# Kernel tuning notes

Hardware: AMD Instinct MI355X
Metric: run time of the kernel (lower is better)

## Reference

```python
import jax, jax.numpy as jnp
import numpy as np

TAU = 2.0      # LIF membrane time constant
V_TH = 1.0     # firing threshold (spikingjelly default)
NUM_HEADS = 8

@jax.custom_vjp
def heaviside(x, alpha):
    return (x >= 0.0).astype(x.dtype)

def _hv_fwd(x, alpha):
    return heaviside(x, alpha), (x, alpha)

def _hv_bwd(res, g):
    x, alpha = res
    s = jax.nn.sigmoid(alpha * x)  # sigmoid surrogate gradient
    return (g * alpha * s * (1.0 - s), jnp.zeros_like(alpha))

heaviside.defvjp(_hv_fwd, _hv_bwd)

def lif(x_seq, alpha):
    """Multi-step LIF over leading time dim. Hard reset to 0, detach_reset."""
    def step(v, x):
        h = v + (x - v) / TAU
        s = heaviside(h - V_TH, alpha)
        v_new = h * (1.0 - jax.lax.stop_gradient(s))
        return v_new, s
    _, spikes = jax.lax.scan(step, jnp.zeros_like(x_seq[0]), x_seq)
    return spikes

def bn1d(x, gamma, beta, mean, var, eps=1e-5):
    # x: [TB, C, N]; inference-mode BatchNorm1d over channel dim
    inv = gamma / jnp.sqrt(var + eps)
    return x * inv[None, :, None] + (beta - mean * inv)[None, :, None]

def setup_inputs():
    T, B, C, H, W = 4, 32, 384, 16, 16
    key = jax.random.key(0)
    ks = jax.random.split(key, 6)
    w = lambda k: jax.random.normal(k, (C, C), jnp.float32) * (1.0 / np.sqrt(C))
    ones = jnp.ones((C,), jnp.float32)
    zeros = jnp.zeros((C,), jnp.float32)
    return dict(
        x=jax.random.normal(ks[0], (T, B, C, H, W), jnp.float32),
        alpha=jnp.float32(2.0),
        q_w=w(ks[1]), q_gamma=ones, q_beta=zeros, q_mean=zeros, q_var=ones,
        k_w=w(ks[2]), k_gamma=ones, k_beta=zeros, k_mean=zeros, k_var=ones,
        v_w=w(ks[3]), v_gamma=ones, v_beta=zeros, v_mean=zeros, v_var=ones,
        proj_w=w(ks[4]), proj_b=jax.random.normal(ks[5], (C,), jnp.float32) * 0.01,
        p_gamma=ones, p_beta=zeros, p_mean=zeros, p_var=ones,
    )

def reference(x, alpha, q_w, q_gamma, q_beta, q_mean, q_var,
              k_w, k_gamma, k_beta, k_mean, k_var,
              v_w, v_gamma, v_beta, v_mean, v_var,
              proj_w, proj_b, p_gamma, p_beta, p_mean, p_var):
    T, B, C, H, W = x.shape
    N = H * W
    d = C // NUM_HEADS

    s = lif(x, alpha).reshape(T, B, C, N)         # proj_lif + flatten(3)
    xf = s.reshape(T * B, C, N)                   # flatten(0,1)

    def branch(w_, g_, b_, m_, v_):
        y = jnp.einsum('oc,bcn->bon', w_, xf)     # conv1x1
        y = bn1d(y, g_, b_, m_, v_).reshape(T, B, C, N)
        y = lif(y, alpha)
        # [T,B,C,N] -> [T,B,N,C] -> [T,B,N,h,d] -> [T,B,h,N,d]
        return y.transpose(0, 1, 3, 2).reshape(T, B, N, NUM_HEADS, d).transpose(0, 1, 3, 2, 4)

    q = branch(q_w, q_gamma, q_beta, q_mean, q_var)
    k = branch(k_w, k_gamma, k_beta, k_mean, k_var)
    v = branch(v_w, v_gamma, v_beta, v_mean, v_var)

    attn = jnp.einsum('tbhnd,tbhmd->tbhnm', q, k)          # q @ k^T (no softmax)
    out = jnp.einsum('tbhnm,tbhmd->tbhnd', attn, v) * 0.125
    # transpose(3,4) then reshape -> [T,B,C,N] (head-major channel layout)
    out = out.transpose(0, 1, 2, 4, 3).reshape(T, B, C, N)
    out = lif(out, alpha)                                  # attn_lif

    of = out.reshape(T * B, C, N)
    y = jnp.einsum('oc,bcn->bon', proj_w, of) + proj_b[None, :, None]
    y = bn1d(y, p_gamma, p_beta, p_mean, p_var)
    return y.reshape(T, B, C, H, W)
```

## Files before the change

### kernel.cpp

```cpp
#include <hip/hip_runtime.h>
#include <hip/hip_bf16.h>

#define T_  4
#define B_  32
#define C_  384
#define N_  256
#define NH_ 8
#define D_  48

typedef __attribute__((ext_vector_type(8))) short bf16x8;
typedef __attribute__((ext_vector_type(4))) float f32x4;

__device__ __forceinline__ float bf2f(unsigned short s) {
    return __uint_as_float(((unsigned int)s) << 16);
}
__device__ __forceinline__ unsigned short f2bf(float f) {
    __hip_bfloat16 h = __float2bfloat16(f);
    return __builtin_bit_cast(unsigned short, h);
}

__global__ __launch_bounds__(256) void k_wsplit(const float* __restrict__ w0,
                                                const float* __restrict__ w1,
                                                const float* __restrict__ w2,
                                                const float* __restrict__ w3,
                                                unsigned short* __restrict__ hi,
                                                unsigned short* __restrict__ lo) {
    const float* w = (blockIdx.y==0) ? w0 : (blockIdx.y==1) ? w1 : (blockIdx.y==2) ? w2 : w3;
    int g = blockIdx.x*256 + threadIdx.x;
    int otile = g / 768;
    int rem = g - otile*768;
    int lane = rem & 63;
    int o  = otile*16 + (lane & 15);
    int k0 = (rem >> 6)*32 + (lane >> 4)*8;
    const float* src = w + (size_t)o*C_ + k0;
    unsigned short h8[8], l8[8];
    #pragma unroll
    for (int j=0;j<8;++j) {
        float f = src[j];
        h8[j] = f2bf(f);
        l8[j] = f2bf(f - bf2f(h8[j]));
    }
    size_t dst = (size_t)blockIdx.y*147456 + (size_t)g*8;
    *(uint4*)(hi + dst) = *(uint4*)h8;
    *(uint4*)(lo + dst) = *(uint4*)l8;
}

__global__ __launch_bounds__(256) void k_lif1(const float* __restrict__ x,
                                              unsigned char* __restrict__ s0b) {
    __shared__ unsigned short Tt[64*72];
    const int tid = threadIdx.x;
    const int b  = blockIdx.x;
    const int c0 = blockIdx.y * 64;
    const int n0 = blockIdx.z * 64;
    const int ci = tid >> 2;
    const int nj = (tid & 3) * 16;
    float v[16];
    #pragma unroll
    for (int i=0;i<16;++i) v[i]=0.f;
    for (int t = 0; t < T_; ++t) {
        const float* xp = x + (((size_t)t*B_ + b)*C_ + c0 + ci)*N_ + n0 + nj;
        #pragma unroll
        for (int q=0;q<4;++q) {
            float4 f = *(const float4*)(xp + q*4);
            float e[4] = {f.x,f.y,f.z,f.w};
            #pragma unroll
            for (int j=0;j<4;++j) {
                int ii = q*4+j;
                float h = v[ii] + (e[j] - v[ii])*0.5f;
                bool sp = (h - 1.0f) >= 0.f;
                v[ii] = sp ? 0.f : h;
                Tt[(nj + ii)*72 + ci] = sp ? 0x3F80u : 0u;
            }
        }
        __syncthreads();
        #pragma unroll
        for (int half=0; half<2; ++half) {
            int e = tid + half*256;
            int nl = e >> 3, cbyte = e & 7;
            unsigned short tmp[8];
            *(uint4*)tmp = *(const uint4*)&Tt[nl*72 + cbyte*8];
            unsigned byte = 0;
            #pragma unroll
            for (int j=0;j<8;++j) byte |= (tmp[j] ? 1u : 0u) << j;
            int n = n0 + nl, c = c0 + cbyte*8;
            int ks = c >> 5, kc = (c >> 3) & 3;
            size_t dst = ((((size_t)(t*B_ + b)*16 + (n>>4))*12 + ks)*64) + kc*16 + (n & 15);
            s0b[dst] = (unsigned char)byte;
        }
        __syncthreads();
    }
}

struct Br2 {
    const unsigned short* whi[3];
    const unsigned short* wlo[3];
    const float *g[3], *be[3], *me[3], *va[3];
    unsigned char* outb[3];
};

__global__ __launch_bounds__(256, 2) void k_branch(const unsigned char* __restrict__ s0b, Br2 a) {
    __shared__ float Ep[32*132];
    __shared__ float BNi[128], BNo[128];
    __shared__ unsigned short LUT[2048];
    const int tid = threadIdx.x;
    const int z  = blockIdx.z;
    const int o0 = blockIdx.y * 128;
    const int bx = blockIdx.x;
    const int b  = bx >> 3;
    const int n0 = (bx & 7) * 32;
    const int g32 = n0 >> 5;
    const int w    = tid >> 6;
    const int lane = tid & 63;
    const int quad = lane >> 4;
    const int lc   = lane & 15;
    const unsigned short* __restrict__ Wgh = a.whi[z];
    const unsigned short* __restrict__ Wgl = a.wlo[z];

    #pragma unroll
    for (int j=0;j<8;++j) LUT[tid*8 + j] = ((tid >> j) & 1) ? 0x3F80u : 0u;
    if (tid < 128) {
        int o = o0 + tid;
        float inv = a.g[z][o] / sqrtf(a.va[z][o] + 1e-5f);
        BNi[tid] = inv;
        BNo[tid] = a.be[z][o] - a.me[z][o]*inv;
    }
    __syncthreads();

    const int base_ot = (o0 >> 4) + (w >> 1)*4;
    const unsigned short* pAh[4];
    const unsigned short* pAl[4];
    const unsigned char* pBY[4];
    #pragma unroll
    for (int mt=0;mt<4;++mt) {
        size_t off = (size_t)(base_ot + mt)*6144 + lane*8;
        pAh[mt] = Wgh + off;
        pAl[mt] = Wgl + off;
    }
    #pragma unroll
    for (int nt=0;nt<4;++nt) {
        int cb = (w&1)*64 + nt*16;
        int t = cb >> 5;
        int ntile = (n0 >> 4) + ((cb >> 4) & 1);
        pBY[nt] = s0b + ((size_t)(t*B_ + b)*16 + ntile)*768 + lane;
    }

    f32x4 acc[4][4];
    #pragma unroll
    for (int mt=0;mt<4;++mt)
        #pragma unroll
        for (int nt=0;nt<4;++nt) { acc[mt][nt][0]=0.f; acc[mt][nt][1]=0.f; acc[mt][nt][2]=0.f; acc[mt][nt][3]=0.f; }

    #pragma unroll
    for (int ks = 0; ks < 12; ++ks) {
        bf16x8 ah[4], al[4], bb[4];
        unsigned char byt[4];
        #pragma unroll
        for (int nt=0;nt<4;++nt) { byt[nt] = *(pBY[nt]); pBY[nt] += 64; }
        #pragma unroll
        for (int mt=0;mt<4;++mt) {
            ah[mt] = *(const bf16x8*)(pAh[mt]); pAh[mt] += 512;
            al[mt] = *(const bf16x8*)(pAl[mt]); pAl[mt] += 512;
        }
        #pragma unroll
        for (int nt=0;nt<4;++nt) bb[nt] = *(const bf16x8*)&LUT[(int)byt[nt]*8];
        #pragma unroll
        for (int mt=0;mt<4;++mt)
            #pragma unroll
            for (int nt=0;nt<4;++nt) {
                acc[mt][nt] = __builtin_amdgcn_mfma_f32_16x16x32_bf16(ah[mt], bb[nt], acc[mt][nt], 0,0,0);
                acc[mt][nt] = __builtin_amdgcn_mfma_f32_16x16x32_bf16(al[mt], bb[nt], acc[mt][nt], 0,0,0);
            }
    }

    unsigned char* outb = a.outb[z];
    for (int r = 0; r < 4; ++r) {
        __syncthreads();
        int erow = (w>>1)*16 + quad*4;
        #pragma unroll
        for (int nt=0;nt<4;++nt) {
            int col = (w&1)*64 + nt*16 + lc;
            Ep[(erow+0)*132 + col] = acc[r][nt][0];
            Ep[(erow+1)*132 + col] = acc[r][nt][1];
            Ep[(erow+2)*132 + col] = acc[r][nt][2];
            Ep[(erow+3)*132 + col] = acc[r][nt][3];
        }
        __syncthreads();
        if (tid < 128) {
            int orow = tid >> 2;
            int bidx = tid & 3;
            int oloc = ((orow & 16) ? 64 : 0) + r*16 + (orow & 15);
            int o = o0 + oloc;
            float inv = BNi[oloc], off = BNo[oloc];
            float v[8];
            #pragma unroll
            for (int j=0;j<8;++j) v[j]=0.f;
            #pragma unroll
            for (int t=0;t<4;++t) {
                float4 f0 = *(const float4*)&Ep[orow*132 + t*32 + bidx*8];
                float4 f1 = *(const float4*)&Ep[orow*132 + t*32 + bidx*8 + 4];
                float e[8] = {f0.x,f0.y,f0.z,f0.w,f1.x,f1.y,f1.z,f1.w};
                unsigned byte = 0;
                #pragma unroll
                for (int j=0;j<8;++j) {
                    float y = e[j]*inv + off;
                    float h = v[j] + (y - v[j])*0.5f;
                    bool sp = (h - 1.0f) >= 0.f;
                    v[j] = sp ? 0.f : h;
                    byte |= (sp ? 1u : 0u) << j;
                }
                outb[(((size_t)(t*B_ + b)*8 + g32)*C_ + o)*4 + bidx] = (unsigned char)byte;
            }
        }
    }
}

__global__ __launch_bounds__(256) void k_attn(const unsigned char* __restrict__ qb,
                                              const unsigned char* __restrict__ kb,
                                              const unsigned char* __restrict__ vb,
                                              unsigned char* __restrict__ s2b) {
    __shared__ unsigned short Qt[256*72];
    __shared__ unsigned short KtVb[48*72];
    __shared__ unsigned long long KB[192], VB[192], QB[192];
    const int tid = threadIdx.x;
    const int w = tid >> 6, lane = tid & 63, quad = lane >> 4, lc = lane & 15;
    const int bh = blockIdx.x;
    const int b  = bh >> 3, hh = bh & 7;

    *(uint4*)&Qt[tid*72 + 48] = make_uint4(0,0,0,0);
    *(uint4*)&Qt[tid*72 + 56] = make_uint4(0,0,0,0);
    if (tid < 48) {
        *(uint4*)&KtVb[tid*72 + 48] = make_uint4(0,0,0,0);
        *(uint4*)&KtVb[tid*72 + 56] = make_uint4(0,0,0,0);
    }

    float vst[4][3][4];
    #pragma unroll
    for (int j=0;j<4;++j)
        #pragma unroll
        for (int nt=0;nt<3;++nt)
            #pragma unroll
            for (int r=0;r<4;++r) vst[j][nt][r]=0.f;

    for (int t = 0; t < T_; ++t) {
        __syncthreads();
        if (tid < 192) {
            int dd = tid >> 2, w64 = tid & 3;
            size_t s0 = (((size_t)(t*B_ + b)*8 + 2*w64)*C_ + hh*D_ + dd)*4;
            size_t s1 = s0 + (size_t)C_*4;
            KB[tid] = (unsigned long long)*(const unsigned int*)(kb + s0)
                    | ((unsigned long long)*(const unsigned int*)(kb + s1) << 32);
            VB[tid] = (unsigned long long)*(const unsigned int*)(vb + s0)
                    | ((unsigned long long)*(const unsigned int*)(vb + s1) << 32);
            QB[tid] = (unsigned long long)*(const unsigned int*)(qb + s0)
                    | ((unsigned long long)*(const unsigned int*)(qb + s1) << 32);
        }
        __syncthreads();
        {
            int q64 = tid >> 6, sh = tid & 63;
            #pragma unroll
            for (int dd=0; dd<48; ++dd)
                Qt[tid*72 + dd] = ((QB[dd*4 + q64] >> sh) & 1ULL) ? 0x3F80u : 0u;
        }
        #pragma unroll
        for (int i=0;i<9;++i) {
            int p = tid + i*256;
            if (p < 2304) {
                int dd1 = p / 48, dd2 = p - dd1*48;
                const unsigned long long* kr = &KB[dd1*4];
                const unsigned long long* vr = &VB[dd2*4];
                int c = __popcll(kr[0]&vr[0]) + __popcll(kr[1]&vr[1])
                      + __popcll(kr[2]&vr[2]) + __popcll(kr[3]&vr[3]);
                KtVb[dd2*72 + dd1] = f2bf((float)c);
            }
        }
        __syncthreads();
        f32x4 acc2[4][3];
        #pragma unroll
        for (int j=0;j<4;++j)
            #pragma unroll
            for (int nt=0;nt<3;++nt) { acc2[j][nt][0]=0.f; acc2[j][nt][1]=0.f; acc2[j][nt][2]=0.f; acc2[j][nt][3]=0.f; }
        #pragma unroll
        for (int k2=0; k2<2; ++k2) {
            bf16x8 bfr[3];
            #pragma unroll
            for (int nt=0;nt<3;++nt)
                bfr[nt] = *(const bf16x8*)&KtVb[(nt*16 + lc)*72 + k2*32 + quad*8];
            #pragma unroll
            for (int j=0;j<4;++j) {
                bf16x8 af = *(const bf16x8*)&Qt[((w*4 + j)*16 + lc)*72 + k2*32 + quad*8];
                #pragma unroll
                for (int nt=0;nt<3;++nt)
                    acc2[j][nt] = __builtin_amdgcn_mfma_f32_16x16x32_bf16(af, bfr[nt], acc2[j][nt], 0,0,0);
            }
        }
        #pragma unroll
        for (int j=0;j<4;++j) {
            int nr = (w*4 + j)*16 + quad*4;
            #pragma unroll
            for (int nt=0;nt<3;++nt)
                #pragma unroll
                for (int r=0;r<4;++r) {
                    float y = acc2[j][nt][r]*0.125f;
                    float vv = vst[j][nt][r];
                    float h = vv + (y - vv)*0.5f;
                    bool s = (h - 1.0f) >= 0.f;
                    vst[j][nt][r] = s ? 0.f : h;
                    Qt[(nr + r)*72 + nt*16 + lc] = s ? 0x3F80u : 0u;
                }
        }
        __syncthreads();
        {
            #pragma unroll
            for (int c8=0; c8<6; ++c8) {
                unsigned short tmp[8];
                *(uint4*)tmp = *(const uint4*)&Qt[tid*72 + c8*8];
                unsigned byte = 0;
                #pragma unroll
                for (int j=0;j<8;++j) byte |= (tmp[j] ? 1u : 0u) << j;
                int ci = hh*6 + c8;
                int ks = ci >> 2, kc = ci & 3;
                size_t dst = ((((size_t)(t*B_ + b)*16 + (tid>>4))*12 + ks)*64) + kc*16 + (tid & 15);
                s2b[dst] = (unsigned char)byte;
            }
        }
    }
}

__global__ __launch_bounds__(256, 2) void k_proj(const unsigned char* __restrict__ s2b,
        const unsigned short* __restrict__ Wgh, const unsigned short* __restrict__ Wgl,
        const float* __restrict__ pb,
        const float* __restrict__ g, const float* __restrict__ be,
        const float* __restrict__ me, const float* __restrict__ va,
        float* __restrict__ out) {
    __shared__ float Ep[32*132];
    __shared__ float BNi[128], BNo[128];
    __shared__ unsigned short LUT[2048];
    const int tid = threadIdx.x;
    const int o0 = blockIdx.y * 128;
    const int bx = blockIdx.x;
    const int t  = bx >> 6;
    const int b  = (bx >> 1) & 31;
    const int n0 = (bx & 1) * 128;
    const int w    = tid >> 6;
    const int lane = tid & 63;
    const int quad = lane >> 4;
    const int lc   = lane & 15;

    #pragma unroll
    for (int j=0;j<8;++j) LUT[tid*8 + j] = ((tid >> j) & 1) ? 0x3F80u : 0u;
    if (tid < 128) {
        int o = o0 + tid;
        float inv = g[o] / sqrtf(va[o] + 1e-5f);
        BNi[tid] = inv;
        BNo[tid] = be[o] - me[o]*inv + pb[o]*inv;
    }
    __syncthreads();

    const int base_ot = (o0 >> 4) + (w >> 1)*4;
    const unsigned short* pAh[4];
    const unsigned short* pAl[4];
    const unsigned char* pBY[4];
    #pragma unroll
    for (int mt=0;mt<4;++mt) {
        size_t off = (size_t)(base_ot + mt)*6144 + lane*8;
        pAh[mt] = Wgh + off;
        pAl[mt] = Wgl + off;
    }
    #pragma unroll
    for (int nt=0;nt<4;++nt) {
        int cb = (w&1)*64 + nt*16;
        int ntile = (n0 >> 4) + (cb >> 4);
        pBY[nt] = s2b + ((size_t)(t*B_ + b)*16 + ntile)*768 + lane;
    }

    f32x4 acc[4][4];
    #pragma unroll
    for (int mt=0;mt<4;++mt)
        #pragma unroll
        for (int nt=0;nt<4;++nt) { acc[mt][nt][0]=0.f; acc[mt][nt][1]=0.f; acc[mt][nt][2]=0.f; acc[mt][nt][3]=0.f; }

    #pragma unroll
    for (int ks = 0; ks < 12; ++ks) {
        bf16x8 ah[4], al[4], bb[4];
        unsigned char byt[4];
        #pragma unroll
        for (int nt=0;nt<4;++nt) { byt[nt] = *(pBY[nt]); pBY[nt] += 64; }
        #pragma unroll
        for (int mt=0;mt<4;++mt) {
            ah[mt] = *(const bf16x8*)(pAh[mt]); pAh[mt] += 512;
            al[mt] = *(const bf16x8*)(pAl[mt]); pAl[mt] += 512;
        }
        #pragma unroll
        for (int nt=0;nt<4;++nt) bb[nt] = *(const bf16x8*)&LUT[(int)byt[nt]*8];
        #pragma unroll
        for (int mt=0;mt<4;++mt)
            #pragma unroll
            for (int nt=0;nt<4;++nt) {
                acc[mt][nt] = __builtin_amdgcn_mfma_f32_16x16x32_bf16(ah[mt], bb[nt], acc[mt][nt], 0,0,0);
                acc[mt][nt] = __builtin_amdgcn_mfma_f32_16x16x32_bf16(al[mt], bb[nt], acc[mt][nt], 0,0,0);
            }
    }

    for (int r = 0; r < 4; ++r) {
        __syncthreads();
        int erow = (w>>1)*16 + quad*4;
        #pragma unroll
        for (int nt=0;nt<4;++nt) {
            int col = (w&1)*64 + nt*16 + lc;
            Ep[(erow+0)*132 + col] = acc[r][nt][0];
            Ep[(erow+1)*132 + col] = acc[r][nt][1];
            Ep[(erow+2)*132 + col] = acc[r][nt][2];
            Ep[(erow+3)*132 + col] = acc[r][nt][3];
        }
        __syncthreads();
        #pragma unroll
        for (int q=0;q<4;++q) {
            int e = q*256 + tid;
            int orow = e >> 5;
            int nq = e & 31;
            int oloc = ((orow & 16) ? 64 : 0) + r*16 + (orow & 15);
            int o = o0 + oloc;
            float4 f = *(const float4*)&Ep[orow*132 + nq*4];
            float inv = BNi[oloc], off = BNo[oloc];
            float4 rr = make_float4(f.x*inv+off, f.y*inv+off, f.z*inv+off, f.w*inv+off);
            *(float4*)(out + (((size_t)t*B_ + b)*C_ + o)*N_ + n0 + nq*4) = rr;
        }
    }
}

extern "C" void kernel_launch(void* const* d_in, const int* in_sizes, int n_in,
                              void* d_out, int out_size, void* d_ws, size_t ws_size,
                              hipStream_t stream) {
    const float* x  = (const float*)d_in[0];
    char* ws = (char*)d_ws;
    unsigned char* S0B = (unsigned char*)ws;
    unsigned char* QB = (unsigned char*)(ws + 2097152);
    unsigned char* KB = (unsigned char*)(ws + 4194304);
    unsigned char* VB = (unsigned char*)(ws + 6291456);
    unsigned char* S2B = (unsigned char*)(ws + 8388608);
    unsigned short* WHI = (unsigned short*)(ws + 100663296);
    unsigned short* WLO = WHI + 4*147456;

    k_wsplit<<<dim3(72,4), 256, 0, stream>>>(
        (const float*)d_in[2], (const float*)d_in[7], (const float*)d_in[12],
        (const float*)d_in[17], WHI, WLO);

    k_lif1<<<dim3(32,6,4), 256, 0, stream>>>(x, S0B);

    Br2 ba;
    for (int z=0;z<3;++z) { ba.whi[z] = WHI + z*147456; ba.wlo[z] = WLO + z*147456; }
    ba.g[0]=(const float*)d_in[3];  ba.be[0]=(const float*)d_in[4];
    ba.me[0]=(const float*)d_in[5]; ba.va[0]=(const float*)d_in[6];
    ba.g[1]=(const float*)d_in[8];  ba.be[1]=(const float*)d_in[9];
    ba.me[1]=(const float*)d_in[10]; ba.va[1]=(const float*)d_in[11];
    ba.g[2]=(const float*)d_in[13]; ba.be[2]=(const float*)d_in[14];
    ba.me[2]=(const float*)d_in[15]; ba.va[2]=(const float*)d_in[16];
    ba.outb[0]=QB; ba.outb[1]=KB; ba.outb[2]=VB;
    k_branch<<<dim3(256, 3, 3), 256, 0, stream>>>(S0B, ba);

    k_attn<<<B_*NH_, 256, 0, stream>>>(QB, KB, VB, S2B);

    k_proj<<<dim3(256, 3), 256, 0, stream>>>(S2B,
        WHI + 3*147456, WLO + 3*147456,
        (const float*)d_in[18],
        (const float*)d_in[19], (const float*)d_in[20],
        (const float*)d_in[21], (const float*)d_in[22],
        (float*)d_out);
}
```

Before: 217.8 us.

## Prefetch next k-step operands in GEMMs, vectorize Qt stores, direct proj epilogue

Both GEMM kernels now double-buffer their weight and spike-byte loads in registers, issuing the loads for step ks+1 before the MFMAs of step ks so memory latency overlaps with compute. The attention kernel builds the Qt bf16 row eight elements at a time and writes it with one 16-byte shared store instead of scalar stores. The projection kernel drops its shared-memory epilogue staging and writes accumulators straight to global memory with BN applied, removing two barriers per row group. The trade-offs are higher register pressure from the prefetch buffers and scalar 4-byte global stores in place of float4 stores.

```diff
diff --git a/kernel.cpp b/kernel.cpp
--- a/kernel.cpp
+++ b/kernel.cpp
@@ -150,26 +150,45 @@
         #pragma unroll
         for (int nt=0;nt<4;++nt) { acc[mt][nt][0]=0.f; acc[mt][nt][1]=0.f; acc[mt][nt][2]=0.f; acc[mt][nt][3]=0.f; }
 
+    unsigned char cby[4];
+    bf16x8 cah[4], cal[4];
+    #pragma unroll
+    for (int nt=0;nt<4;++nt) { cby[nt] = *(pBY[nt]); pBY[nt] += 64; }
+    #pragma unroll
+    for (int mt=0;mt<4;++mt) {
+        cah[mt] = *(const bf16x8*)(pAh[mt]); pAh[mt] += 512;
+        cal[mt] = *(const bf16x8*)(pAl[mt]); pAl[mt] += 512;
+    }
+
     #pragma unroll
     for (int ks = 0; ks < 12; ++ks) {
-        bf16x8 ah[4], al[4], bb[4];
-        unsigned char byt[4];
-        #pragma unroll
-        for (int nt=0;nt<4;++nt) { byt[nt] = *(pBY[nt]); pBY[nt] += 64; }
-        #pragma unroll
-        for (int mt=0;mt<4;++mt) {
-            ah[mt] = *(const bf16x8*)(pAh[mt]); pAh[mt] += 512;
-            al[mt] = *(const bf16x8*)(pAl[mt]); pAl[mt] += 512;
-        }
-        #pragma unroll
-        for (int nt=0;nt<4;++nt) bb[nt] = *(const bf16x8*)&LUT[(int)byt[nt]*8];
+        unsigned char nby[4];
+        bf16x8 nah[4], nal[4];
+        if (ks < 11) {
+            #pragma unroll
+            for (int nt=0;nt<4;++nt) { nby[nt] = *(pBY[nt]); pBY[nt] += 64; }
+            #pragma unroll
+            for (int mt=0;mt<4;++mt) {
+                nah[mt] = *(const bf16x8*)(pAh[mt]); pAh[mt] += 512;
+                nal[mt] = *(const bf16x8*)(pAl[mt]); pAl[mt] += 512;
+            }
+        }
+        bf16x8 bb[4];
+        #pragma unroll
+        for (int nt=0;nt<4;++nt) bb[nt] = *(const bf16x8*)&LUT[(int)cby[nt]*8];
         #pragma unroll
         for (int mt=0;mt<4;++mt)
             #pragma unroll
             for (int nt=0;nt<4;++nt) {
-                acc[mt][nt] = __builtin_amdgcn_mfma_f32_16x16x32_bf16(ah[mt], bb[nt], acc[mt][nt], 0,0,0);
-                acc[mt][nt] = __builtin_amdgcn_mfma_f32_16x16x32_bf16(al[mt], bb[nt], acc[mt][nt], 0,0,0);
-            }
+                acc[mt][nt] = __builtin_amdgcn_mfma_f32_16x16x32_bf16(cah[mt], bb[nt], acc[mt][nt], 0,0,0);
+                acc[mt][nt] = __builtin_amdgcn_mfma_f32_16x16x32_bf16(cal[mt], bb[nt], acc[mt][nt], 0,0,0);
+            }
+        if (ks < 11) {
+            #pragma unroll
+            for (int nt=0;nt<4;++nt) cby[nt]=nby[nt];
+            #pragma unroll
+            for (int mt=0;mt<4;++mt) { cah[mt]=nah[mt]; cal[mt]=nal[mt]; }
+        }
     }
 
     unsigned char* outb = a.outb[z];
@@ -258,8 +277,13 @@
         {
             int q64 = tid >> 6, sh = tid & 63;
             #pragma unroll
-            for (int dd=0; dd<48; ++dd)
-                Qt[tid*72 + dd] = ((QB[dd*4 + q64] >> sh) & 1ULL) ? 0x3F80u : 0u;
+            for (int c8=0; c8<6; ++c8) {
+                unsigned short e8[8];
+                #pragma unroll
+                for (int j=0;j<8;++j)
+                    e8[j] = ((QB[(c8*8+j)*4 + q64] >> sh) & 1ULL) ? 0x3F80u : 0u;
+                *(uint4*)&Qt[tid*72 + c8*8] = *(uint4*)e8;
+            }
         }
         #pragma unroll
         for (int i=0;i<9;++i) {
@@ -332,7 +356,6 @@
         const float* __restrict__ g, const float* __restrict__ be,
         const float* __restrict__ me, const float* __restrict__ va,
         float* __restrict__ out) {
-    __shared__ float Ep[32*132];
     __shared__ float BNi[128], BNo[128];
     __shared__ unsigned short LUT[2048];
     const int tid = threadIdx.x;
@@ -379,51 +402,59 @@
         #pragma unroll
         for (int nt=0;nt<4;++nt) { acc[mt][nt][0]=0.f; acc[mt][nt][1]=0.f; acc[mt][nt][2]=0.f; acc[mt][nt][3]=0.f; }
 
+    unsigned char cby[4];
+    bf16x8 cah[4], cal[4];
+    #pragma unroll
+    for (int nt=0;nt<4;++nt) { cby[nt] = *(pBY[nt]); pBY[nt] += 64; }
+    #pragma unroll
+    for (int mt=0;mt<4;++mt) {
+        cah[mt] = *(const bf16x8*)(pAh[mt]); pAh[mt] += 512;
+        cal[mt] = *(const bf16x8*)(pAl[mt]); pAl[mt] += 512;
+    }
+
     #pragma unroll
     for (int ks = 0; ks < 12; ++ks) {
-        bf16x8 ah[4], al[4], bb[4];
-        unsigned char byt[4];
-        #pragma unroll
-        for (int nt=0;nt<4;++nt) { byt[nt] = *(pBY[nt]); pBY[nt] += 64; }
-        #pragma unroll
-        for (int mt=0;mt<4;++mt) {
-            ah[mt] = *(const bf16x8*)(pAh[mt]); pAh[mt] += 512;
-            al[mt] = *(const bf16x8*)(pAl[mt]); pAl[mt] += 512;
-        }
-        #pragma unroll
-        for (int nt=0;nt<4;++nt) bb[nt] = *(const bf16x8*)&LUT[(int)byt[nt]*8];
+        unsigned char nby[4];
+        bf16x8 nah[4], nal[4];
+        if (ks < 11) {
+            #pragma unroll
+            for (int nt=0;nt<4;++nt) { nby[nt] = *(pBY[nt]); pBY[nt] += 64; }
+            #pragma unroll
+            for (int mt=0;mt<4;++mt) {
+                nah[mt] = *(const bf16x8*)(pAh[mt]); pAh[mt] += 512;
+                nal[mt] = *(const bf16x8*)(pAl[mt]); pAl[mt] += 512;
+            }
+        }
+        bf16x8 bb[4];
+        #pragma unroll
+        for (int nt=0;nt<4;++nt) bb[nt] = *(const bf16x8*)&LUT[(int)cby[nt]*8];
         #pragma unroll
         for (int mt=0;mt<4;++mt)
             #pragma unroll
             for (int nt=0;nt<4;++nt) {
-                acc[mt][nt] = __builtin_amdgcn_mfma_f32_16x16x32_bf16(ah[mt], bb[nt], acc[mt][nt], 0,0,0);
-                acc[mt][nt] = __builtin_amdgcn_mfma_f32_16x16x32_bf16(al[mt], bb[nt], acc[mt][nt], 0,0,0);
-            }
-    }
-
-    for (int r = 0; r < 4; ++r) {
-        __syncthreads();
-        int erow = (w>>1)*16 + quad*4;
-        #pragma unroll
-        for (int nt=0;nt<4;++nt) {
-            int col = (w&1)*64 + nt*16 + lc;
-            Ep[(erow+0)*132 + col] = acc[r][nt][0];
-            Ep[(erow+1)*132 + col] = acc[r][nt][1];
-            Ep[(erow+2)*132 + col] = acc[r][nt][2];
-            Ep[(erow+3)*132 + col] = acc[r][nt][3];
-        }
-        __syncthreads();
-        #pragma unroll
-        for (int q=0;q<4;++q) {
-            int e = q*256 + tid;
-            int orow = e >> 5;
-            int nq = e & 31;
-            int oloc = ((orow & 16) ? 64 : 0) + r*16 + (orow & 15);
+                acc[mt][nt] = __builtin_amdgcn_mfma_f32_16x16x32_bf16(cah[mt], bb[nt], acc[mt][nt], 0,0,0);
+                acc[mt][nt] = __builtin_amdgcn_mfma_f32_16x16x32_bf16(cal[mt], bb[nt], acc[mt][nt], 0,0,0);
+            }
+        if (ks < 11) {
+            #pragma unroll
+            for (int nt=0;nt<4;++nt) cby[nt]=nby[nt];
+            #pragma unroll
+            for (int mt=0;mt<4;++mt) { cah[mt]=nah[mt]; cal[mt]=nal[mt]; }
+        }
+    }
+
+    float* obase = out + ((size_t)t*B_ + b)*C_*N_;
+    #pragma unroll
+    for (int mt=0;mt<4;++mt) {
+        #pragma unroll
+        for (int r=0;r<4;++r) {
+            int oloc = (w>>1)*64 + mt*16 + quad*4 + r;
             int o = o0 + oloc;
-            float4 f = *(const float4*)&Ep[orow*132 + nq*4];
             float inv = BNi[oloc], off = BNo[oloc];
-            float4 rr = make_float4(f.x*inv+off, f.y*inv+off, f.z*inv+off, f.w*inv+off);
-            *(float4*)(out + (((size_t)t*B_ + b)*C_ + o)*N_ + n0 + nq*4) = rr;
+            float* orow = obase + (size_t)o*N_ + n0 + (w&1)*64 + lc;
+            #pragma unroll
+            for (int nt=0;nt<4;++nt)
+                orow[nt*16] = acc[mt][nt][r]*inv + off;
         }
     }
 }
```

Result: slower. 276.1 us (+26.7%).
